# Optimization experiments

Measured on AMD Instinct MI355X. Metric: run time of the kernel, lower is better.

Reference implementation:

```python
import jax, jax.numpy as jnp
import numpy as np

B = 32
H = W = 64
C = 128
HEADS = 4
HEAD_DIM = C // HEADS
WS = 8            # window_size
SS = 4            # shift_size
N = WS * WS       # tokens per window
MLP_HID = 4 * C
SCALE = HEAD_DIM ** -0.5
EPS = 1e-5


def _rel_pos_index():
    coords = np.stack(np.meshgrid(np.arange(WS), np.arange(WS), indexing='ij'))
    cf = coords.reshape(2, -1)
    rel = (cf[:, :, None] - cf[:, None, :]).transpose(1, 2, 0)
    rel[:, :, 0] += WS - 1
    rel[:, :, 1] += WS - 1
    rel[:, :, 0] *= 2 * WS - 1
    return rel.sum(-1)  # (N, N) int


def _attn_mask():
    img_mask = np.zeros((1, H, W, 1), np.float32)
    slices = (slice(0, -WS), slice(-WS, -SS), slice(-SS, None))
    cnt = 0
    for hs in slices:
        for ws in slices:
            img_mask[:, hs, ws, :] = cnt
            cnt += 1
    mw = img_mask.reshape(1, H // WS, WS, W // WS, WS, 1)
    mw = mw.transpose(0, 1, 3, 2, 4, 5).reshape(-1, N)  # (nW, N)
    am = mw[:, None, :] - mw[:, :, None]
    return np.where(am != 0, np.float32(-100.0), np.float32(0.0))  # (nW, N, N)


REL_POS_IDX = jnp.asarray(_rel_pos_index().reshape(-1))  # (N*N,)
ATTN_MASK = jnp.asarray(_attn_mask())                    # (nW, N, N)


def setup_inputs() -> dict:
    key = jax.random.key(0)
    ks = jax.random.split(key, 12)
    s = 0.02
    return {
        'x': jax.random.normal(ks[0], (B, H * W, C), jnp.float32),
        'norm1_g': jnp.ones((C,), jnp.float32),
        'norm1_b': jnp.zeros((C,), jnp.float32),
        'qkv_w': jax.random.normal(ks[1], (C, 3 * C), jnp.float32) * s,
        'qkv_b': jnp.zeros((3 * C,), jnp.float32),
        'proj_w': jax.random.normal(ks[2], (C, C), jnp.float32) * s,
        'proj_b': jnp.zeros((C,), jnp.float32),
        'rpb_table': jax.random.normal(ks[3], ((2 * WS - 1) * (2 * WS - 1), HEADS), jnp.float32) * s,
        'norm2_g': jnp.ones((C,), jnp.float32),
        'norm2_b': jnp.zeros((C,), jnp.float32),
        'mlp_w1': jax.random.normal(ks[4], (C, MLP_HID), jnp.float32) * s,
        'mlp_b1': jnp.zeros((MLP_HID,), jnp.float32),
        'mlp_w2': jax.random.normal(ks[5], (MLP_HID, C), jnp.float32) * s,
        'mlp_b2': jnp.zeros((C,), jnp.float32),
    }


def _layernorm(x, g, b):
    m = x.mean(-1, keepdims=True)
    v = jnp.mean((x - m) ** 2, -1, keepdims=True)
    return (x - m) * jax.lax.rsqrt(v + EPS) * g + b


def reference(x, norm1_g, norm1_b, qkv_w, qkv_b, proj_w, proj_b, rpb_table,
              norm2_g, norm2_b, mlp_w1, mlp_b1, mlp_w2, mlp_b2):
    shortcut = x
    h = _layernorm(x, norm1_g, norm1_b).reshape(-1, H, W, C)
    # cyclic shift
    h = jnp.roll(h, (-SS, -SS), axis=(1, 2))
    # window partition -> (B*nW, N, C)
    hw = h.reshape(-1, H // WS, WS, W // WS, WS, C)
    hw = hw.transpose(0, 1, 3, 2, 4, 5).reshape(-1, N, C)
    # window attention
    qkv = (hw @ qkv_w + qkv_b).reshape(-1, N, 3, HEADS, HEAD_DIM)
    qkv = qkv.transpose(2, 0, 3, 1, 4)  # (3, B*nW, heads, N, hd)
    q, k, v = qkv[0] * SCALE, qkv[1], qkv[2]
    attn = jnp.einsum('bhnd,bhmd->bhnm', q, k)  # (B*nW, heads, N, N)
    rpb = rpb_table[REL_POS_IDX].reshape(N, N, HEADS).transpose(2, 0, 1)
    attn = attn + rpb[None]
    nW = ATTN_MASK.shape[0]
    attn = attn.reshape(-1, nW, HEADS, N, N) + ATTN_MASK[None, :, None]
    attn = jax.nn.softmax(attn.reshape(-1, HEADS, N, N), axis=-1)
    out = jnp.einsum('bhnm,bhmd->bhnd', attn, v)
    out = out.transpose(0, 2, 1, 3).reshape(-1, N, C)
    out = out @ proj_w + proj_b
    # window reverse
    out = out.reshape(-1, H // WS, W // WS, WS, WS, C)
    out = out.transpose(0, 1, 3, 2, 4, 5).reshape(-1, H, W, C)
    # reverse cyclic shift
    out = jnp.roll(out, (SS, SS), axis=(1, 2)).reshape(-1, H * W, C)
    x = shortcut + out
    # MLP branch
    h2 = _layernorm(x, norm2_g, norm2_b)
    h2 = jax.nn.gelu(h2 @ mlp_w1 + mlp_b1, approximate=False)
    h2 = h2 @ mlp_w2 + mlp_b2
    return x + h2
```

## Files before the change

kernel.cpp:

```cpp
#include <hip/hip_runtime.h>
#include <math.h>

typedef __attribute__((ext_vector_type(8))) short bf16x8;
typedef __attribute__((ext_vector_type(4))) short bf16x4;
typedef __attribute__((ext_vector_type(4))) float f32x4;
typedef __attribute__((ext_vector_type(4))) unsigned short u16x4;

#define DEVI __device__ __forceinline__

DEVI float b2f(unsigned int u){ union{unsigned int i; float f;} c; c.i = u<<16; return c.f; }
DEVI unsigned short f2b(float f){
  union{float f; unsigned int i;} c; c.f = f;
  unsigned int r = c.i + 0x7fffu + ((c.i>>16)&1u);
  return (unsigned short)(r>>16);
}
DEVI unsigned int pack2(float a, float b){
  return (unsigned int)f2b(a) | ((unsigned int)f2b(b)<<16);
}
DEVI void unpack8(uint4 u, float* f){
  f[0]=b2f(u.x&0xffffu); f[1]=b2f(u.x>>16);
  f[2]=b2f(u.y&0xffffu); f[3]=b2f(u.y>>16);
  f[4]=b2f(u.z&0xffffu); f[5]=b2f(u.z>>16);
  f[6]=b2f(u.w&0xffffu); f[7]=b2f(u.w>>16);
}
DEVI f32x4 mfma16(bf16x8 a, bf16x8 b, f32x4 c){
  return __builtin_amdgcn_mfma_f32_16x16x32_bf16(a, b, c, 0, 0, 0);
}
DEVI f32x4 mfma16x16(bf16x4 a, bf16x4 b, f32x4 c){
#if __has_builtin(__builtin_amdgcn_mfma_f32_16x16x16bf16_1k)
  return __builtin_amdgcn_mfma_f32_16x16x16bf16_1k(a, b, c, 0, 0, 0);
#else
  f32x4 d = c;
  asm volatile("v_mfma_f32_16x16x16_bf16 %0, %1, %2, %0" : "+v"(d) : "v"(a), "v"(b));
  return d;
#endif
}
DEVI float gelu_fast(float u){
  const float y = 0.7978845608028654f*(u + 0.044715f*u*u*u);
  const float t = __expf(2.f*y);
  const float th = 1.f - 2.f/(t + 1.f);
  return 0.5f*u*(1.f + th);
}
DEVI int swzA(int row, int byi){ return row*256 + (byi ^ ((row&7)<<4)); }
DEVI int swzQ(int row, int byi){ return row*64  + (byi ^ (((row>>1)&3)<<4)); }
DEVI int swzP(int row, int byi){ return row*128 + (byi ^ ((row&7)<<4)); }

__global__ void k_prep(const float* __restrict__ qkvw, const float* __restrict__ projw,
                       const float* __restrict__ w1,   const float* __restrict__ w2,
                       ushort* __restrict__ qkvF, ushort* __restrict__ projF,
                       ushort* __restrict__ w1F,  ushort* __restrict__ w2F)
{
  const int t = blockIdx.x*256 + threadIdx.x;
  const int l = t&63, fr = t>>6;
  const int l15 = l&15, l4 = l>>4;
  {
    const int c = fr>>5, og = (fr>>2)&7, h = fr&3;
    const int oc = og*16 + l15, hid0 = c*64 + h*16 + l4*4;
    ushort* d = w2F + (size_t)fr*256 + l*4;
    #pragma unroll
    for(int e=0;e<4;e++) d[e] = f2b(w2[(size_t)(hid0+e)*128 + oc]);
  }
  if (fr < 128){
    const int c = fr>>4, hg = (fr>>2)&3, kk = fr&3;
    const int hid = c*64 + hg*16 + l15, k0 = kk*32 + l4*8;
    ushort* d = w1F + (size_t)fr*512 + l*8;
    #pragma unroll
    for(int e=0;e<8;e++) d[e] = f2b(w1[(size_t)(k0+e)*512 + hid]);
  }
  if (fr < 96){
    const int s3 = fr>>5, g = (fr>>2)&7, kk = fr&3;
    const int col = s3*128 + g*16 + l15, k0 = kk*32 + l4*8;
    ushort* d = qkvF + (size_t)fr*512 + l*8;
    #pragma unroll
    for(int e=0;e<8;e++) d[e] = f2b(qkvw[(size_t)(k0+e)*384 + col]);
  }
  if (fr < 32){
    const int g = fr>>2, kk = fr&3;
    const int col = g*16 + l15, k0 = kk*32 + l4*8;
    ushort* d = projF + (size_t)fr*512 + l*8;
    #pragma unroll
    for(int e=0;e<8;e++) d[e] = f2b(projw[(size_t)(k0+e)*128 + col]);
  }
}

__global__ __launch_bounds__(256,2) void k_attn(
    const float*  __restrict__ x,
    const float*  __restrict__ g1, const float* __restrict__ be1,
    const ushort* __restrict__ qkvF, const float* __restrict__ qkvb,
    const ushort* __restrict__ projF, const float* __restrict__ projb,
    const float*  __restrict__ rpbt,
    ushort* __restrict__ x2w)
{
  __shared__ __align__(16) char smem[65536];
  const int tid  = threadIdx.x;
  const int wave = tid>>6, lane = tid&63;
  const int l15 = lane&15, l4 = lane>>4;
  const int wid = blockIdx.x;
  const int b   = wid>>6, wim = wid&63;
  const int wh  = wim>>3, wv = wim&7;

  char* const smA  = smem;
  char* const smHd = smem + 16384 + wave*12288;
  char* const smQ  = smHd;
  char* const smK  = smHd + 4096;
  char* const smVT = smHd + 8192;
  char* const smP  = smHd;

  const f32x4 Z = {0.f,0.f,0.f,0.f};

  {
    const int t  = tid>>2;
    const int cg = (tid&3)*32;
    const int ti = t>>3, tj = t&7;
    const int ho = (wh*8+ti+4)&63, wo = (wv*8+tj+4)&63;
    const float* src = x + ((size_t)(b*4096 + ho*64 + wo))*128 + cg;
    float v[32];
    #pragma unroll
    for(int q=0;q<8;q++){
      const float4 f4 = *(const float4*)(src + q*4);
      v[q*4+0]=f4.x; v[q*4+1]=f4.y; v[q*4+2]=f4.z; v[q*4+3]=f4.w;
    }
    float s=0.f, ss=0.f;
    #pragma unroll
    for(int e=0;e<32;e++){ s+=v[e]; ss+=v[e]*v[e]; }
    s += __shfl_xor(s,1); ss += __shfl_xor(ss,1);
    s += __shfl_xor(s,2); ss += __shfl_xor(ss,2);
    const float mean = s*(1.f/128.f);
    const float varv = fmaxf(ss*(1.f/128.f) - mean*mean, 0.f);
    const float rstd = rsqrtf(varv + 1e-5f);
    #pragma unroll
    for(int q=0;q<4;q++){
      const float4 ga = *(const float4*)(g1 +cg+q*8);
      const float4 gb = *(const float4*)(g1 +cg+q*8+4);
      const float4 ba = *(const float4*)(be1+cg+q*8);
      const float4 bb = *(const float4*)(be1+cg+q*8+4);
      const float* vp = v + q*8;
      uint4 pk;
      pk.x = pack2((vp[0]-mean)*rstd*ga.x+ba.x, (vp[1]-mean)*rstd*ga.y+ba.y);
      pk.y = pack2((vp[2]-mean)*rstd*ga.z+ba.z, (vp[3]-mean)*rstd*ga.w+ba.w);
      pk.z = pack2((vp[4]-mean)*rstd*gb.x+bb.x, (vp[5]-mean)*rstd*gb.y+bb.y);
      pk.w = pack2((vp[6]-mean)*rstd*gb.z+bb.z, (vp[7]-mean)*rstd*gb.w+bb.w);
      *(uint4*)(smA + swzA(t, cg*2 + q*16)) = pk;
    }
  }
  __syncthreads();

  const int headc = wave*32;
  {
    #pragma unroll
    for(int s3=0;s3<3;s3++){
      f32x4 acc[4][2];
      #pragma unroll
      for(int rt=0;rt<4;rt++){ acc[rt][0]=Z; acc[rt][1]=Z; }
      bf16x8 bfr[2][4];
      #pragma unroll
      for(int ct=0;ct<2;ct++)
        #pragma unroll
        for(int kk=0;kk<4;kk++)
          bfr[ct][kk] = *(const bf16x8*)(qkvF + (size_t)((s3*8 + wave*2 + ct)*4 + kk)*512 + lane*8);
      #pragma unroll
      for(int kk=0;kk<4;kk++){
        bf16x8 afr[4];
        #pragma unroll
        for(int rt=0;rt<4;rt++)
          afr[rt] = *(const bf16x8*)(smA + swzA(rt*16+l15, kk*64 + l4*16));
        #pragma unroll
        for(int rt=0;rt<4;rt++)
          #pragma unroll
          for(int ct=0;ct<2;ct++)
            acc[rt][ct] = mfma16(afr[rt], bfr[ct][kk], acc[rt][ct]);
      }
      #pragma unroll
      for(int ct=0;ct<2;ct++){
        const int hd = ct*16 + l15;
        const float bias = qkvb[s3*128 + headc + hd];
        #pragma unroll
        for(int rt=0;rt<4;rt++){
          const int t0 = rt*16 + l4*4;
          if (s3==2){
            uint2 pk;
            pk.x = pack2(acc[rt][ct][0]+bias, acc[rt][ct][1]+bias);
            pk.y = pack2(acc[rt][ct][2]+bias, acc[rt][ct][3]+bias);
            *(uint2*)(smVT + swzP(hd, t0*2)) = pk;
          } else {
            char* const dst = (s3==0) ? smQ : smK;
            const float sc = (s3==0) ? 0.17677669529663687f : 1.f;
            #pragma unroll
            for(int j=0;j<4;j++)
              *(ushort*)(dst + swzQ(t0+j, hd*2)) = f2b((acc[rt][ct][j]+bias)*sc);
          }
        }
      }
    }
  }
  __syncthreads();

  {
    f32x4 S[4][4];
    bf16x8 qfr[4], kfr[4];
    #pragma unroll
    for(int i=0;i<4;i++) qfr[i] = *(const bf16x8*)(smQ + swzQ(i*16+l15, l4*16));
    #pragma unroll
    for(int i=0;i<4;i++) kfr[i] = *(const bf16x8*)(smK + swzQ(i*16+l15, l4*16));
    #pragma unroll
    for(int rt=0;rt<4;rt++)
      #pragma unroll
      for(int ct=0;ct<4;ct++)
        S[rt][ct] = mfma16(qfr[rt], kfr[ct], Z);

    const bool edge = (wh==7) || (wv==7);
    #pragma unroll
    for(int ct=0;ct<4;ct++){
      const int m = ct*16 + l15;
      const int im = m>>3, jm = m&7;
      const int regm = ((wh<7)?0:((im<4)?1:2))*3 + ((wv<7)?0:((jm<4)?1:2));
      #pragma unroll
      for(int rt=0;rt<4;rt++)
        #pragma unroll
        for(int j=0;j<4;j++){
          const int n = rt*16 + l4*4 + j;
          const int in_ = n>>3, jn = n&7;
          float add = rpbt[((in_-im+7)*15 + (jn-jm+7))*4 + wave];
          if (edge){
            const int regn = ((wh<7)?0:((in_<4)?1:2))*3 + ((wv<7)?0:((jn<4)?1:2));
            if (regn != regm) add -= 100.f;
          }
          S[rt][ct][j] += add;
        }
    }
    #pragma unroll
    for(int rt=0;rt<4;rt++)
      #pragma unroll
      for(int j=0;j<4;j++){
        float mx = fmaxf(fmaxf(S[rt][0][j],S[rt][1][j]), fmaxf(S[rt][2][j],S[rt][3][j]));
        mx = fmaxf(mx, __shfl_xor(mx,1));
        mx = fmaxf(mx, __shfl_xor(mx,2));
        mx = fmaxf(mx, __shfl_xor(mx,4));
        mx = fmaxf(mx, __shfl_xor(mx,8));
        float sm = 0.f;
        #pragma unroll
        for(int ct=0;ct<4;ct++){ const float e = __expf(S[rt][ct][j]-mx); S[rt][ct][j]=e; sm+=e; }
        sm += __shfl_xor(sm,1);
        sm += __shfl_xor(sm,2);
        sm += __shfl_xor(sm,4);
        sm += __shfl_xor(sm,8);
        const float inv = 1.f/sm;
        #pragma unroll
        for(int ct=0;ct<4;ct++) S[rt][ct][j] *= inv;
      }
    #pragma unroll
    for(int rt=0;rt<4;rt++)
      #pragma unroll
      for(int j=0;j<4;j++){
        const int n = rt*16 + l4*4 + j;
        #pragma unroll
        for(int ct=0;ct<4;ct++)
          *(ushort*)(smP + swzP(n, (ct*16+l15)*2)) = f2b(S[rt][ct][j]);
      }
  }

  {
    f32x4 O[4][2];
    #pragma unroll
    for(int rt=0;rt<4;rt++){ O[rt][0]=Z; O[rt][1]=Z; }
    #pragma unroll
    for(int kk=0;kk<2;kk++){
      bf16x8 pfr[4], vfr[2];
      #pragma unroll
      for(int rt=0;rt<4;rt++)
        pfr[rt] = *(const bf16x8*)(smP + swzP(rt*16+l15, kk*64 + l4*16));
      #pragma unroll
      for(int ct=0;ct<2;ct++)
        vfr[ct] = *(const bf16x8*)(smVT + swzP(ct*16+l15, kk*64 + l4*16));
      #pragma unroll
      for(int rt=0;rt<4;rt++)
        #pragma unroll
        for(int ct=0;ct<2;ct++)
          O[rt][ct] = mfma16(pfr[rt], vfr[ct], O[rt][ct]);
    }
    #pragma unroll
    for(int rt=0;rt<4;rt++)
      #pragma unroll
      for(int ct=0;ct<2;ct++)
        #pragma unroll
        for(int j=0;j<4;j++){
          const int t = rt*16 + l4*4 + j;
          *(ushort*)(smA + swzA(t, (headc + ct*16 + l15)*2)) = f2b(O[rt][ct][j]);
        }
  }
  __syncthreads();

  {
    f32x4 PR[4][2];
    #pragma unroll
    for(int rt=0;rt<4;rt++){ PR[rt][0]=Z; PR[rt][1]=Z; }
    bf16x8 pb[2][4];
    #pragma unroll
    for(int ct=0;ct<2;ct++)
      #pragma unroll
      for(int kk=0;kk<4;kk++)
        pb[ct][kk] = *(const bf16x8*)(projF + (size_t)((wave*2+ct)*4 + kk)*512 + lane*8);
    #pragma unroll
    for(int kk=0;kk<4;kk++){
      bf16x8 afr[4];
      #pragma unroll
      for(int rt=0;rt<4;rt++)
        afr[rt] = *(const bf16x8*)(smA + swzA(rt*16+l15, kk*64 + l4*16));
      #pragma unroll
      for(int rt=0;rt<4;rt++)
        #pragma unroll
        for(int ct=0;ct<2;ct++)
          PR[rt][ct] = mfma16(afr[rt], pb[ct][kk], PR[rt][ct]);
    }
    #pragma unroll
    for(int ct=0;ct<2;ct++){
      const int col = headc + ct*16 + l15;
      const float bias = projb[col];
      #pragma unroll
      for(int rt=0;rt<4;rt++)
        #pragma unroll
        for(int j=0;j<4;j++){
          const int t = rt*16 + l4*4 + j;
          const int ti = t>>3, tj = t&7;
          const int ho = (wh*8+ti+4)&63, wo = (wv*8+tj+4)&63;
          const float sc = x[((size_t)(b*4096 + ho*64 + wo))*128 + col];
          x2w[((size_t)(wid*64 + t))*128 + col] = f2b(PR[rt][ct][j] + bias + sc);
        }
    }
  }
}

__global__ __launch_bounds__(512,1) void k_mlp2(
    const ushort* __restrict__ x2w,
    const float* __restrict__ g2, const float* __restrict__ be2,
    const ushort* __restrict__ w1F, const float* __restrict__ bb1,
    const ushort* __restrict__ w2F, const float* __restrict__ bb2,
    float* __restrict__ outp)
{
  extern __shared__ __align__(16) char smem[];
  char* const smX  = smem;
  char* const smW0 = smem + 65536;
  char* const smW1 = smem + 98304;
  const int tid  = threadIdx.x;
  const int wave = tid>>6, lane = tid&63;
  const int l15 = lane&15, l4 = lane>>4;
  const int gblk = blockIdx.x;
  const f32x4 Z = {0.f,0.f,0.f,0.f};

  const ushort* const wsrc = (tid & 256) ? w2F : w1F;
  const int soff = (tid & 255) * 32;
  const int loff = ((tid & 256) ? 16384 : 0) + (tid & 255)*64;
  uint4 stg0, stg1, stg2, stg3;
  {
    const uint4* p = (const uint4*)(wsrc + soff);
    stg0 = p[0]; stg1 = p[1]; stg2 = p[2]; stg3 = p[3];
  }

  {
    const int sub = tid>>2;
    const int cg  = (tid&3)*32;
    #pragma unroll
    for(int p=0;p<2;++p){
      const int tk = p*128 + sub;
      const ushort* src = x2w + ((size_t)(gblk*256 + tk))*128 + cg;
      float v[32];
      unpack8(*(const uint4*)(src   ), v   );
      unpack8(*(const uint4*)(src+ 8), v+ 8);
      unpack8(*(const uint4*)(src+16), v+16);
      unpack8(*(const uint4*)(src+24), v+24);
      float s=0.f, ss=0.f;
      #pragma unroll
      for(int e=0;e<32;e++){ s+=v[e]; ss+=v[e]*v[e]; }
      s += __shfl_xor(s,1); ss += __shfl_xor(ss,1);
      s += __shfl_xor(s,2); ss += __shfl_xor(ss,2);
      const float mean = s*(1.f/128.f);
      const float varv = fmaxf(ss*(1.f/128.f) - mean*mean, 0.f);
      const float rstd = rsqrtf(varv + 1e-5f);
      #pragma unroll
      for(int q=0;q<4;q++){
        const float4 ga = *(const float4*)(g2 +cg+q*8);
        const float4 gb = *(const float4*)(g2 +cg+q*8+4);
        const float4 ba = *(const float4*)(be2+cg+q*8);
        const float4 bb = *(const float4*)(be2+cg+q*8+4);
        const float* vp = v + q*8;
        uint4 pk;
        pk.x = pack2((vp[0]-mean)*rstd*ga.x+ba.x, (vp[1]-mean)*rstd*ga.y+ba.y);
        pk.y = pack2((vp[2]-mean)*rstd*ga.z+ba.z, (vp[3]-mean)*rstd*ga.w+ba.w);
        pk.z = pack2((vp[4]-mean)*rstd*gb.x+bb.x, (vp[5]-mean)*rstd*gb.y+bb.y);
        pk.w = pack2((vp[6]-mean)*rstd*gb.z+bb.z, (vp[7]-mean)*rstd*gb.w+bb.w);
        *(uint4*)(smX + swzA(tk, cg*2 + q*16)) = pk;
      }
    }
  }
  {
    uint4* d = (uint4*)(smW0 + loff);
    d[0]=stg0; d[1]=stg1; d[2]=stg2; d[3]=stg3;
  }
  __syncthreads();

  f32x4 OA[8][2];
  #pragma unroll
  for(int ocg=0;ocg<8;++ocg){ OA[ocg][0]=Z; OA[ocg][1]=Z; }

  for (int c=0; c<8; ++c){
    char* const buf = (c&1) ? smW1 : smW0;
    if (c<7){
      const uint4* p = (const uint4*)(wsrc + (size_t)(c+1)*8192 + soff);
      stg0 = p[0]; stg1 = p[1]; stg2 = p[2]; stg3 = p[3];
    }
    const int hidb = c*64;
    #pragma unroll
    for (int tokg=0; tokg<2; ++tokg){
      const int trow = wave*32 + tokg*16 + l15;
      bf16x8 xf[4];
      #pragma unroll
      for(int kk=0;kk<4;++kk)
        xf[kk] = *(const bf16x8*)(smX + swzA(trow, kk*64 + l4*16));
      f32x4 acc1[4] = {Z,Z,Z,Z};
      #pragma unroll
      for(int hg=0; hg<4; ++hg)
        #pragma unroll
        for(int kk=0; kk<4; ++kk){
          const bf16x8 wf = *(const bf16x8*)(buf + (hg*4+kk)*1024 + lane*16);
          acc1[hg] = mfma16(wf, xf[kk], acc1[hg]);
        }
      bf16x4 Hf[4];
      #pragma unroll
      for(int hg=0; hg<4; ++hg){
        const float4 b4 = *(const float4*)(bb1 + hidb + hg*16 + l4*4);
        bf16x4 hv;
        hv[0] = (short)f2b(gelu_fast(acc1[hg][0]+b4.x));
        hv[1] = (short)f2b(gelu_fast(acc1[hg][1]+b4.y));
        hv[2] = (short)f2b(gelu_fast(acc1[hg][2]+b4.z));
        hv[3] = (short)f2b(gelu_fast(acc1[hg][3]+b4.w));
        Hf[hg] = hv;
      }
      #pragma unroll
      for(int ocg=0; ocg<8; ++ocg)
        #pragma unroll
        for(int hg=0; hg<4; ++hg){
          const bf16x4 w2f = *(const bf16x4*)(buf + 16384 + (ocg*4+hg)*512 + lane*8);
          OA[ocg][tokg] = mfma16x16(w2f, Hf[hg], OA[ocg][tokg]);
        }
    }
    if (c<7){
      char* const nbuf = (c&1) ? smW0 : smW1;
      uint4* d = (uint4*)(nbuf + loff);
      d[0]=stg0; d[1]=stg1; d[2]=stg2; d[3]=stg3;
    }
    __syncthreads();
  }

  {
    const int sub = tid>>2;
    const int cg  = (tid&3)*32;
    #pragma unroll
    for(int p=0;p<2;++p){
      const int tk = p*128 + sub;
      const uint4* src = (const uint4*)(x2w + ((size_t)(gblk*256 + tk))*128 + cg);
      #pragma unroll
      for(int q=0;q<4;q++) *(uint4*)(smX + swzA(tk, cg*2 + q*16)) = src[q];
    }
  }
  __syncthreads();
  #pragma unroll
  for(int tokg=0; tokg<2; ++tokg){
    const int tk  = wave*32 + tokg*16 + l15;
    const int wid = gblk*4 + (tk>>6);
    const int n   = tk & 63;
    const int bb  = wid>>6, wim = wid&63;
    const int wh  = wim>>3, wv = wim&7;
    const int ti  = n>>3,  tj = n&7;
    const int ho  = (wh*8+ti+4)&63, wo = (wv*8+tj+4)&63;
    float* const drow = outp + ((size_t)(bb*4096 + ho*64 + wo))*128;
    #pragma unroll
    for(int ocg=0; ocg<8; ++ocg){
      const int oc = ocg*16 + l4*4;
      const float4 b4 = *(const float4*)(bb2 + oc);
      const u16x4 xr = *(const u16x4*)(smX + swzA(tk, oc*2));
      f32x4 r = OA[ocg][tokg];
      r[0] += b4.x + b2f(xr[0]);
      r[1] += b4.y + b2f(xr[1]);
      r[2] += b4.z + b2f(xr[2]);
      r[3] += b4.w + b2f(xr[3]);
      __builtin_nontemporal_store(r, (f32x4*)(drow + oc));
    }
  }
}

extern "C" void kernel_launch(void* const* d_in, const int* in_sizes, int n_in,
                              void* d_out, int out_size, void* d_ws, size_t ws_size,
                              hipStream_t stream) {
  (void)in_sizes; (void)n_in; (void)out_size; (void)ws_size;
  const float* x     = (const float*)d_in[0];
  const float* n1g   = (const float*)d_in[1];
  const float* n1b   = (const float*)d_in[2];
  const float* qkvw  = (const float*)d_in[3];
  const float* qkvb  = (const float*)d_in[4];
  const float* projw = (const float*)d_in[5];
  const float* projb = (const float*)d_in[6];
  const float* rpbt  = (const float*)d_in[7];
  const float* n2g   = (const float*)d_in[8];
  const float* n2b   = (const float*)d_in[9];
  const float* w1    = (const float*)d_in[10];
  const float* b1    = (const float*)d_in[11];
  const float* w2    = (const float*)d_in[12];
  const float* b2    = (const float*)d_in[13];
  float* outp = (float*)d_out;

  ushort* ws    = (ushort*)d_ws;
  ushort* x2w   = ws;
  ushort* qkvF  = ws + 16777216;
  ushort* projF = qkvF + 49152;
  ushort* w1F   = projF + 16384;
  ushort* w2F   = w1F + 65536;

  k_prep<<<64, 256, 0, stream>>>(qkvw, projw, w1, w2, qkvF, projF, w1F, w2F);
  k_attn<<<2048, 256, 0, stream>>>(x, n1g, n1b, qkvF, qkvb, projF, projb, rpbt, x2w);
  k_mlp2<<<512, 512, 131072, stream>>>(x2w, n2g, n2b, w1F, b1, w2F, b2, outp);
}
```

Baseline: 210.0 us.

## Keep P and V in registers, pre-expand rel-pos bias, stage residual via LDS

Computes S transposed (K·Q) so the softmax output is already in the MFMA A-operand layout and feeds the PV product straight from registers. V also stays in registers, which removes the P and V^T shared-memory round trips and cuts LDS to 48KB, so occupancy is raised to 3 blocks per CU. The relative-position bias is pre-expanded to a bf16 per-head 64x64 table in k_prep, replacing per-element gathers. The projection output is staged through swizzled LDS so the residual add and the bf16 store become coalesced vector accesses. The trade-offs are higher register pressure and bias rounded to bf16.

```diff
diff --git a/kernel.cpp b/kernel.cpp
--- a/kernel.cpp
+++ b/kernel.cpp
@@ -43,17 +43,24 @@
 }
 DEVI int swzA(int row, int byi){ return row*256 + (byi ^ ((row&7)<<4)); }
 DEVI int swzQ(int row, int byi){ return row*64  + (byi ^ (((row>>1)&3)<<4)); }
-DEVI int swzP(int row, int byi){ return row*128 + (byi ^ ((row&7)<<4)); }
+DEVI int swzO(int row, int byc){ return row*512 + (byc ^ ((row&7)<<4) ^ (((byc>>7)&3)<<5)); }
 
 __global__ void k_prep(const float* __restrict__ qkvw, const float* __restrict__ projw,
                        const float* __restrict__ w1,   const float* __restrict__ w2,
+                       const float* __restrict__ rpbt,
                        ushort* __restrict__ qkvF, ushort* __restrict__ projF,
-                       ushort* __restrict__ w1F,  ushort* __restrict__ w2F)
+                       ushort* __restrict__ w1F,  ushort* __restrict__ w2F,
+                       ushort* __restrict__ rpbE)
 {
   const int t = blockIdx.x*256 + threadIdx.x;
   const int l = t&63, fr = t>>6;
   const int l15 = l&15, l4 = l>>4;
   {
+    const int head = t>>12, q = (t>>6)&63, k = t&63;
+    const int di = (q>>3)-(k>>3)+7, dj = (q&7)-(k&7)+7;
+    rpbE[t] = f2b(rpbt[(di*15+dj)*4 + head]);
+  }
+  {
     const int c = fr>>5, og = (fr>>2)&7, h = fr&3;
     const int oc = og*16 + l15, hid0 = c*64 + h*16 + l4*4;
     ushort* d = w2F + (size_t)fr*256 + l*4;
@@ -83,15 +90,15 @@
   }
 }
 
-__global__ __launch_bounds__(256,2) void k_attn(
+__global__ __launch_bounds__(256,3) void k_attn(
     const float*  __restrict__ x,
     const float*  __restrict__ g1, const float* __restrict__ be1,
     const ushort* __restrict__ qkvF, const float* __restrict__ qkvb,
     const ushort* __restrict__ projF, const float* __restrict__ projb,
-    const float*  __restrict__ rpbt,
+    const ushort* __restrict__ rpbE,
     ushort* __restrict__ x2w)
 {
-  __shared__ __align__(16) char smem[65536];
+  __shared__ __align__(16) char smem[49152];
   const int tid  = threadIdx.x;
   const int wave = tid>>6, lane = tid&63;
   const int l15 = lane&15, l4 = lane>>4;
@@ -100,20 +107,19 @@
   const int wh  = wim>>3, wv = wim&7;
 
   char* const smA  = smem;
-  char* const smHd = smem + 16384 + wave*12288;
-  char* const smQ  = smHd;
-  char* const smK  = smHd + 4096;
-  char* const smVT = smHd + 8192;
-  char* const smP  = smHd;
+  char* const smQ  = smem + 16384 + wave*8192;
+  char* const smK  = smQ + 4096;
+  char* const smR  = smem + 16384;
 
   const f32x4 Z = {0.f,0.f,0.f,0.f};
-
-  {
-    const int t  = tid>>2;
-    const int cg = (tid&3)*32;
-    const int ti = t>>3, tj = t&7;
-    const int ho = (wh*8+ti+4)&63, wo = (wv*8+tj+4)&63;
-    const float* src = x + ((size_t)(b*4096 + ho*64 + wo))*128 + cg;
+  const int t_row = tid>>2;
+  const int cg    = (tid&3)*32;
+  const int ti_r = t_row>>3, tj_r = t_row&7;
+  const int ho_r = (wh*8+ti_r+4)&63, wo_r = (wv*8+tj_r+4)&63;
+  const size_t growbase = ((size_t)(b*4096 + ho_r*64 + wo_r))*128;
+
+  {
+    const float* src = x + growbase + cg;
     float v[32];
     #pragma unroll
     for(int q=0;q<8;q++){
@@ -140,12 +146,14 @@
       pk.y = pack2((vp[2]-mean)*rstd*ga.z+ba.z, (vp[3]-mean)*rstd*ga.w+ba.w);
       pk.z = pack2((vp[4]-mean)*rstd*gb.x+bb.x, (vp[5]-mean)*rstd*gb.y+bb.y);
       pk.w = pack2((vp[6]-mean)*rstd*gb.z+bb.z, (vp[7]-mean)*rstd*gb.w+bb.w);
-      *(uint4*)(smA + swzA(t, cg*2 + q*16)) = pk;
+      *(uint4*)(smA + swzA(t_row, cg*2 + q*16)) = pk;
     }
   }
   __syncthreads();
 
   const int headc = wave*32;
+  bf16x4 Vf[4][2];
+
   {
     #pragma unroll
     for(int s3=0;s3<3;s3++){
@@ -174,17 +182,20 @@
       for(int ct=0;ct<2;ct++){
         const int hd = ct*16 + l15;
         const float bias = qkvb[s3*128 + headc + hd];
-        #pragma unroll
-        for(int rt=0;rt<4;rt++){
-          const int t0 = rt*16 + l4*4;
-          if (s3==2){
-            uint2 pk;
-            pk.x = pack2(acc[rt][ct][0]+bias, acc[rt][ct][1]+bias);
-            pk.y = pack2(acc[rt][ct][2]+bias, acc[rt][ct][3]+bias);
-            *(uint2*)(smVT + swzP(hd, t0*2)) = pk;
-          } else {
-            char* const dst = (s3==0) ? smQ : smK;
-            const float sc = (s3==0) ? 0.17677669529663687f : 1.f;
+        if (s3==2){
+          #pragma unroll
+          for(int rt=0;rt<4;rt++){
+            union { uint2 u; bf16x4 v; } cv;
+            cv.u.x = pack2(acc[rt][ct][0]+bias, acc[rt][ct][1]+bias);
+            cv.u.y = pack2(acc[rt][ct][2]+bias, acc[rt][ct][3]+bias);
+            Vf[rt][ct] = cv.v;
+          }
+        } else {
+          char* const dst = (s3==0) ? smQ : smK;
+          const float sc = (s3==0) ? 0.17677669529663687f : 1.f;
+          #pragma unroll
+          for(int rt=0;rt<4;rt++){
+            const int t0 = rt*16 + l4*4;
             #pragma unroll
             for(int j=0;j<4;j++)
               *(ushort*)(dst + swzQ(t0+j, hd*2)) = f2b((acc[rt][ct][j]+bias)*sc);
@@ -195,98 +206,76 @@
   }
   __syncthreads();
 
-  {
-    f32x4 S[4][4];
-    bf16x8 qfr[4], kfr[4];
-    #pragma unroll
-    for(int i=0;i<4;i++) qfr[i] = *(const bf16x8*)(smQ + swzQ(i*16+l15, l4*16));
-    #pragma unroll
-    for(int i=0;i<4;i++) kfr[i] = *(const bf16x8*)(smK + swzQ(i*16+l15, l4*16));
+  f32x4 O[4][2];
+  #pragma unroll
+  for(int rt=0;rt<4;rt++){ O[rt][0]=Z; O[rt][1]=Z; }
+  {
+    bf16x8 kfr[4];
+    #pragma unroll
+    for(int g=0; g<4; ++g)
+      kfr[g] = *(const bf16x8*)(smK + swzQ(g*16+l15, l4*16));
+    const bool edge = (wh==7) || (wv==7);
+    #pragma unroll
+    for(int rt=0; rt<4; ++rt){
+      const bf16x8 qf = *(const bf16x8*)(smQ + swzQ(rt*16+l15, l4*16));
+      f32x4 S[4];
+      #pragma unroll
+      for(int g=0; g<4; ++g)
+        S[g] = mfma16(kfr[g], qf, Z);
+      const int q = rt*16 + l15;
+      int regq = 0;
+      if (edge){
+        const int qi=q>>3, qj=q&7;
+        regq = ((wh<7)?0:((qi<4)?1:2))*3 + ((wv<7)?0:((qj<4)?1:2));
+      }
+      const ushort* rbase = rpbE + wave*4096 + q*64 + l4*4;
+      #pragma unroll
+      for(int g=0; g<4; ++g){
+        const u16x4 rb = *(const u16x4*)(rbase + g*16);
+        #pragma unroll
+        for(int j=0;j<4;j++){
+          float add = b2f(rb[j]);
+          if (edge){
+            const int k = g*16 + l4*4 + j;
+            const int ki=k>>3, kj=k&7;
+            const int regk = ((wh<7)?0:((ki<4)?1:2))*3 + ((wv<7)?0:((kj<4)?1:2));
+            if (regk != regq) add -= 100.f;
+          }
+          S[g][j] += add;
+        }
+      }
+      float mx = -1e30f;
+      #pragma unroll
+      for(int g=0;g<4;g++)
+        #pragma unroll
+        for(int j=0;j<4;j++) mx = fmaxf(mx, S[g][j]);
+      mx = fmaxf(mx, __shfl_xor(mx,16));
+      mx = fmaxf(mx, __shfl_xor(mx,32));
+      float sm = 0.f;
+      #pragma unroll
+      for(int g=0;g<4;g++)
+        #pragma unroll
+        for(int j=0;j<4;j++){ const float e = __expf(S[g][j]-mx); S[g][j]=e; sm+=e; }
+      sm += __shfl_xor(sm,16);
+      sm += __shfl_xor(sm,32);
+      const float inv = 1.f/sm;
+      #pragma unroll
+      for(int g=0;g<4;g++){
+        union { uint2 u; bf16x4 v; } cv;
+        cv.u.x = pack2(S[g][0]*inv, S[g][1]*inv);
+        cv.u.y = pack2(S[g][2]*inv, S[g][3]*inv);
+        #pragma unroll
+        for(int cvi=0;cvi<2;cvi++)
+          O[rt][cvi] = mfma16x16(cv.v, Vf[g][cvi], O[rt][cvi]);
+      }
+    }
     #pragma unroll
     for(int rt=0;rt<4;rt++)
       #pragma unroll
-      for(int ct=0;ct<4;ct++)
-        S[rt][ct] = mfma16(qfr[rt], kfr[ct], Z);
-
-    const bool edge = (wh==7) || (wv==7);
-    #pragma unroll
-    for(int ct=0;ct<4;ct++){
-      const int m = ct*16 + l15;
-      const int im = m>>3, jm = m&7;
-      const int regm = ((wh<7)?0:((im<4)?1:2))*3 + ((wv<7)?0:((jm<4)?1:2));
-      #pragma unroll
-      for(int rt=0;rt<4;rt++)
-        #pragma unroll
-        for(int j=0;j<4;j++){
-          const int n = rt*16 + l4*4 + j;
-          const int in_ = n>>3, jn = n&7;
-          float add = rpbt[((in_-im+7)*15 + (jn-jm+7))*4 + wave];
-          if (edge){
-            const int regn = ((wh<7)?0:((in_<4)?1:2))*3 + ((wv<7)?0:((jn<4)?1:2));
-            if (regn != regm) add -= 100.f;
-          }
-          S[rt][ct][j] += add;
-        }
-    }
-    #pragma unroll
-    for(int rt=0;rt<4;rt++)
-      #pragma unroll
-      for(int j=0;j<4;j++){
-        float mx = fmaxf(fmaxf(S[rt][0][j],S[rt][1][j]), fmaxf(S[rt][2][j],S[rt][3][j]));
-        mx = fmaxf(mx, __shfl_xor(mx,1));
-        mx = fmaxf(mx, __shfl_xor(mx,2));
-        mx = fmaxf(mx, __shfl_xor(mx,4));
-        mx = fmaxf(mx, __shfl_xor(mx,8));
-        float sm = 0.f;
-        #pragma unroll
-        for(int ct=0;ct<4;ct++){ const float e = __expf(S[rt][ct][j]-mx); S[rt][ct][j]=e; sm+=e; }
-        sm += __shfl_xor(sm,1);
-        sm += __shfl_xor(sm,2);
-        sm += __shfl_xor(sm,4);
-        sm += __shfl_xor(sm,8);
-        const float inv = 1.f/sm;
-        #pragma unroll
-        for(int ct=0;ct<4;ct++) S[rt][ct][j] *= inv;
-      }
-    #pragma unroll
-    for(int rt=0;rt<4;rt++)
-      #pragma unroll
-      for(int j=0;j<4;j++){
-        const int n = rt*16 + l4*4 + j;
-        #pragma unroll
-        for(int ct=0;ct<4;ct++)
-          *(ushort*)(smP + swzP(n, (ct*16+l15)*2)) = f2b(S[rt][ct][j]);
-      }
-  }
-
-  {
-    f32x4 O[4][2];
-    #pragma unroll
-    for(int rt=0;rt<4;rt++){ O[rt][0]=Z; O[rt][1]=Z; }
-    #pragma unroll
-    for(int kk=0;kk<2;kk++){
-      bf16x8 pfr[4], vfr[2];
-      #pragma unroll
-      for(int rt=0;rt<4;rt++)
-        pfr[rt] = *(const bf16x8*)(smP + swzP(rt*16+l15, kk*64 + l4*16));
-      #pragma unroll
-      for(int ct=0;ct<2;ct++)
-        vfr[ct] = *(const bf16x8*)(smVT + swzP(ct*16+l15, kk*64 + l4*16));
-      #pragma unroll
-      for(int rt=0;rt<4;rt++)
-        #pragma unroll
-        for(int ct=0;ct<2;ct++)
-          O[rt][ct] = mfma16(pfr[rt], vfr[ct], O[rt][ct]);
-    }
-    #pragma unroll
-    for(int rt=0;rt<4;rt++)
-      #pragma unroll
-      for(int ct=0;ct<2;ct++)
-        #pragma unroll
-        for(int j=0;j<4;j++){
-          const int t = rt*16 + l4*4 + j;
-          *(ushort*)(smA + swzA(t, (headc + ct*16 + l15)*2)) = f2b(O[rt][ct][j]);
-        }
+      for(int cvi=0;cvi<2;cvi++)
+        #pragma unroll
+        for(int j=0;j<4;j++)
+          *(ushort*)(smA + swzA(rt*16+l4*4+j, (headc + cvi*16 + l15)*2)) = f2b(O[rt][cvi][j]);
   }
   __syncthreads();
 
@@ -319,13 +308,27 @@
       #pragma unroll
       for(int rt=0;rt<4;rt++)
         #pragma unroll
-        for(int j=0;j<4;j++){
-          const int t = rt*16 + l4*4 + j;
-          const int ti = t>>3, tj = t&7;
-          const int ho = (wh*8+ti+4)&63, wo = (wv*8+tj+4)&63;
-          const float sc = x[((size_t)(b*4096 + ho*64 + wo))*128 + col];
-          x2w[((size_t)(wid*64 + t))*128 + col] = f2b(PR[rt][ct][j] + bias + sc);
-        }
+        for(int j=0;j<4;j++)
+          *(float*)(smR + swzO(rt*16+l4*4+j, col*4)) = PR[rt][ct][j] + bias;
+    }
+  }
+  __syncthreads();
+
+  {
+    const float* xsrc = x + growbase + cg;
+    ushort* drow = x2w + ((size_t)(wid*64 + t_row))*128 + cg;
+    #pragma unroll
+    for(int q=0;q<4;q++){
+      const f32x4 oa = *(const f32x4*)(smR + swzO(t_row, (cg+q*8  )*4));
+      const f32x4 ob = *(const f32x4*)(smR + swzO(t_row, (cg+q*8+4)*4));
+      const float4 xa = *(const float4*)(xsrc + q*8);
+      const float4 xb = *(const float4*)(xsrc + q*8+4);
+      uint4 pk;
+      pk.x = pack2(oa[0]+xa.x, oa[1]+xa.y);
+      pk.y = pack2(oa[2]+xa.z, oa[3]+xa.w);
+      pk.z = pack2(ob[0]+xb.x, ob[1]+xb.y);
+      pk.w = pack2(ob[2]+xb.z, ob[3]+xb.w);
+      *(uint4*)(drow + q*8) = pk;
     }
   }
 }
@@ -514,8 +517,9 @@
   ushort* projF = qkvF + 49152;
   ushort* w1F   = projF + 16384;
   ushort* w2F   = w1F + 65536;
-
-  k_prep<<<64, 256, 0, stream>>>(qkvw, projw, w1, w2, qkvF, projF, w1F, w2F);
-  k_attn<<<2048, 256, 0, stream>>>(x, n1g, n1b, qkvF, qkvb, projF, projb, rpbt, x2w);
+  ushort* rpbE  = w2F + 65536;
+
+  k_prep<<<64, 256, 0, stream>>>(qkvw, projw, w1, w2, rpbt, qkvF, projF, w1F, w2F, rpbE);
+  k_attn<<<2048, 256, 0, stream>>>(x, n1g, n1b, qkvF, qkvb, projF, projb, rpbE, x2w);
   k_mlp2<<<512, 512, 131072, stream>>>(x2w, n2g, n2b, w1F, b1, w2F, b2, outp);
 }
```

After: 188.1 us. -10.4%, faster.
